# Kernel tuning notes

Hardware: AMD Instinct MI355X
Metric: run time of the kernel (lower is better)

## Reference

```python
import jax, jax.numpy as jnp
import numpy as np

A0, A1, A2 = 1.0, 1.0, 0.5
TEMPERATURE = 1.0

B, H, N, D = 2, 8, 1024, 64


def setup_inputs() -> dict:
    key = jax.random.key(0)
    k1, k2, k3, k4, k5 = jax.random.split(key, 5)
    q = jax.random.normal(k1, (B, H, N, D), dtype=jnp.float32)
    k = jax.random.normal(k2, (B, H, N, D), dtype=jnp.float32)
    v = jax.random.normal(k3, (B, H, N, D), dtype=jnp.float32)
    drop_noise = jax.random.normal(k4, (B, H, N, D), dtype=jnp.float32)
    rpe_matrix = jax.random.normal(k5, (2 * N - 1, D), dtype=jnp.float32)
    return {"q": q, "k": k, "v": v, "drop_noise": drop_noise, "rpe_matrix": rpe_matrix}


def reference(q, k, v, drop_noise, rpe_matrix):
    # Degree-2 Taylor approximation of softmax attention (fastmax):
    #   score_ij = a0 + a1*s_ij + a2*s_ij^2,  s_ij = q_i . k_j + q_i . rpe[i-j+n-1]
    #   o_i = sum_j score_ij * v_j / sum_j score_ij
    # Defaults: mask=False (bidirectional), dropout=0.0 (drop_noise unused),
    # normalize=False, temperature=1.0.
    b, h, n, d = q.shape
    qf = q.reshape(b * h, n, d)
    kf = (k / TEMPERATURE).reshape(b * h, n, d)
    vf = v.reshape(b * h, n, d)

    # dot-product term: (bh, n, n)
    qk = jnp.einsum('bid,bjd->bij', qf, kf)

    # RPE term: P[b,i,r] = q_i . rpe[r]; gather r = i - j + n - 1
    P = jnp.einsum('bid,rd->bir', qf, rpe_matrix)  # (bh, n, 2n-1)
    rel = jnp.arange(n)[:, None] - jnp.arange(n)[None, :] + (n - 1)  # (n, n)
    rel = jnp.broadcast_to(rel[None], (b * h, n, n))
    qk = qk + jnp.take_along_axis(P, rel, axis=2)

    s = A0 + A1 * qk + A2 * qk * qk  # Taylor kernel scores

    denom = jnp.sum(s, axis=-1, keepdims=True)  # (bh, n, 1)
    o = jnp.einsum('bij,bjd->bid', s, vf) / denom
    return o.reshape(b, h, n, d)
```

## Files before the change

kernel.cpp:

```cpp
#include <hip/hip_runtime.h>
#include <hip/hip_bf16.h>


#define NSEQ 1024
#define DH   64
#define BM   64
#define BN   64
#define NBH  16
#define ROWS_TOTAL (NBH * NSEQ)
#define NUM_ELEMS  ((size_t)ROWS_TOTAL * DH)

typedef short bf16x8 __attribute__((ext_vector_type(8)));
typedef float f32x4  __attribute__((ext_vector_type(4)));

__device__ __forceinline__ unsigned short f2bf(float x) {
    return __builtin_bit_cast(unsigned short, __float2bfloat16(x));
}
__device__ __forceinline__ unsigned pack2(float lo, float hi) {
    return (unsigned)f2bf(lo) | ((unsigned)f2bf(hi) << 16);
}
__device__ __forceinline__ unsigned long long pack4(float4 x) {
    unsigned lo = pack2(x.x, x.y), hi = pack2(x.z, x.w);
    return (unsigned long long)lo | ((unsigned long long)hi << 32);
}

template<int JSPLIT>
__global__ __launch_bounds__(512, 2)
void fastmax_kernel(const float* __restrict__ qg, const float* __restrict__ kg,
                    const float* __restrict__ vg, const float* __restrict__ rpe,
                    float* __restrict__ outg, float* __restrict__ wsbuf)
{
    __shared__ __align__(16) unsigned char ldsK[64 * 128];
    __shared__ __align__(16) unsigned char ldsR[128 * 128];
    __shared__ __align__(16) unsigned char ldsVT[64 * 136];
    __shared__ __align__(16) unsigned char ldsS[8 * 16 * 80];

    const int tid = threadIdx.x;
    const int w   = tid >> 6;
    const int l   = tid & 63;
    const int lr  = l & 15;
    const int lg  = l >> 4;
    const int wst = w >> 1;
    const int wj  = w & 1;

    const int b  = blockIdx.x;
    const int js = b % JSPLIT;
    const int it = (b / JSPLIT) & 15;
    const int bh = b / (JSPLIT * 16);
    const int i0 = it * BM;

    const float* qbh = qg + (size_t)bh * (NSEQ * DH);
    const float* kbh = kg + (size_t)bh * (NSEQ * DH);
    const float* vbh = vg + (size_t)bh * (NSEQ * DH);

    bf16x8 qf[2];
    {
        const float* qrow = qbh + (size_t)(i0 + wst * 16 + lr) * DH + lg * 8;
        #pragma unroll
        for (int kc = 0; kc < 2; ++kc) {
            float4 a  = *reinterpret_cast<const float4*>(qrow + kc * 32);
            float4 b4 = *reinterpret_cast<const float4*>(qrow + kc * 32 + 4);
            bf16x8 f;
            f[0] = (short)f2bf(a.x);  f[1] = (short)f2bf(a.y);
            f[2] = (short)f2bf(a.z);  f[3] = (short)f2bf(a.w);
            f[4] = (short)f2bf(b4.x); f[5] = (short)f2bf(b4.y);
            f[6] = (short)f2bf(b4.z); f[7] = (short)f2bf(b4.w);
            qf[kc] = f;
        }
    }

    f32x4 oacc[4];
    #pragma unroll
    for (int dt = 0; dt < 4; ++dt) oacc[dt] = (f32x4){0.f, 0.f, 0.f, 0.f};
    float dp[4] = {0.f, 0.f, 0.f, 0.f};

    unsigned char* myS = ldsS + w * (16 * 80);
    const int t0w = wst * 16 - wj * 32 + 32;

    constexpr int NJT = (NSEQ / BN) / JSPLIT;
    for (int jt = js * NJT; jt < (js + 1) * NJT; ++jt) {
        const int j0  = jt * BN;
        const int rlo = i0 - j0 + 960;

        __syncthreads();

        {
            const float4* src = reinterpret_cast<const float4*>(kbh + (size_t)j0 * DH);
            #pragma unroll
            for (int itr = 0; itr < 2; ++itr) {
                int i = itr * 512 + tid;
                float4 x = src[i];
                int row = i >> 4, colb = (i & 15) * 8;
                *reinterpret_cast<unsigned long long*>(
                    ldsK + ((row * 128 + colb) ^ ((row & 7) << 4))) = pack4(x);
            }
        }
        {
            #pragma unroll
            for (int itr = 0; itr < 4; ++itr) {
                int i = itr * 512 + tid;
                int row = i >> 4;
                int r = rlo + row; if (r > 2 * NSEQ - 2) r = 2 * NSEQ - 2;
                float4 x = reinterpret_cast<const float4*>(rpe)[r * 16 + (i & 15)];
                int colb = (i & 15) * 8;
                *reinterpret_cast<unsigned long long*>(
                    ldsR + ((row * 128 + colb) ^ ((row & 7) << 4))) = pack4(x);
            }
        }
        {
            const float4* src = reinterpret_cast<const float4*>(vbh + (size_t)j0 * DH);
            #pragma unroll
            for (int itr = 0; itr < 2; ++itr) {
                int i = itr * 512 + tid;
                float4 x = src[i];
                int j = i >> 4, d0 = (i & 15) * 4;
                unsigned char* p = ldsVT + j * 2;
                *reinterpret_cast<unsigned short*>(p + (d0 + 0) * 136) = f2bf(x.x);
                *reinterpret_cast<unsigned short*>(p + (d0 + 1) * 136) = f2bf(x.y);
                *reinterpret_cast<unsigned short*>(p + (d0 + 2) * 136) = f2bf(x.z);
                *reinterpret_cast<unsigned short*>(p + (d0 + 3) * 136) = f2bf(x.w);
            }
        }
        __syncthreads();

        f32x4 pacc[3];
        #pragma unroll
        for (int ct = 0; ct < 3; ++ct) pacc[ct] = (f32x4){0.f, 0.f, 0.f, 0.f};
        #pragma unroll
        for (int kc = 0; kc < 2; ++kc) {
            #pragma unroll
            for (int ct = 0; ct < 3; ++ct) {
                int row = t0w + ct * 16 + lr;
                bf16x8 bfrag = *reinterpret_cast<const bf16x8*>(
                    ldsR + ((row * 128 + kc * 64 + lg * 16) ^ ((row & 7) << 4)));
                pacc[ct] = __builtin_amdgcn_mfma_f32_16x16x32_bf16(qf[kc], bfrag, pacc[ct], 0, 0, 0);
            }
        }

        f32x4 sacc[2];
        #pragma unroll
        for (int ct = 0; ct < 2; ++ct) sacc[ct] = (f32x4){0.f, 0.f, 0.f, 0.f};
        #pragma unroll
        for (int kc = 0; kc < 2; ++kc) {
            #pragma unroll
            for (int ct = 0; ct < 2; ++ct) {
                int row = wj * 32 + ct * 16 + lr;
                bf16x8 bfrag = *reinterpret_cast<const bf16x8*>(
                    ldsK + ((row * 128 + kc * 64 + lg * 16) ^ ((row & 7) << 4)));
                sacc[ct] = __builtin_amdgcn_mfma_f32_16x16x32_bf16(qf[kc], bfrag, sacc[ct], 0, 0, 0);
            }
        }

        #pragma unroll
        for (int r = 0; r < 4; ++r) {
            int m = lg * 4 + r;
            int idx = ((l & 48) + ((m - lr + 15) & 15)) << 2;
            int g0 = __builtin_amdgcn_ds_bpermute(idx, __float_as_int(pacc[0][r]));
            int g1 = __builtin_amdgcn_ds_bpermute(idx, __float_as_int(pacc[1][r]));
            int g2 = __builtin_amdgcn_ds_bpermute(idx, __float_as_int(pacc[2][r]));
            bool hi = (m > lr);
            float p0 = __int_as_float(hi ? g2 : g1);
            float p1 = __int_as_float(hi ? g1 : g0);
            float s0 = sacc[0][r] + p0;
            float c0 = fmaf(s0, fmaf(0.5f, s0, 1.0f), 1.0f);
            dp[r] += c0;
            *reinterpret_cast<unsigned short*>(myS + m * 80 + lr * 2) = f2bf(c0);
            float s1 = sacc[1][r] + p1;
            float c1 = fmaf(s1, fmaf(0.5f, s1, 1.0f), 1.0f);
            dp[r] += c1;
            *reinterpret_cast<unsigned short*>(myS + m * 80 + 32 + lr * 2) = f2bf(c1);
        }

        bf16x8 af = *reinterpret_cast<const bf16x8*>(myS + lr * 80 + lg * 16);
        #pragma unroll
        for (int dt = 0; dt < 4; ++dt) {
            const unsigned char* vp = ldsVT + (dt * 16 + lr) * 136 + wj * 64 + lg * 16;
            union { unsigned long long u[2]; bf16x8 v; } bb;
            bb.u[0] = *reinterpret_cast<const unsigned long long*>(vp);
            bb.u[1] = *reinterpret_cast<const unsigned long long*>(vp + 8);
            oacc[dt] = __builtin_amdgcn_mfma_f32_16x16x32_bf16(af, bb.v, oacc[dt], 0, 0, 0);
        }
    }

    #pragma unroll
    for (int r = 0; r < 4; ++r) {
        #pragma unroll
        for (int m = 1; m < 16; m <<= 1) dp[r] += __shfl_xor(dp[r], m, 64);
    }

    if constexpr (JSPLIT == 1) {
        __syncthreads();
        float* ored = reinterpret_cast<float*>(ldsR);
        float* dred = reinterpret_cast<float*>(ldsK);
        if (wj == 1) {
            #pragma unroll
            for (int dt = 0; dt < 4; ++dt) {
                #pragma unroll
                for (int r = 0; r < 4; ++r) {
                    int row = lg * 4 + r;
                    ored[wst * 1024 + row * 64 + dt * 16 + lr] = oacc[dt][r];
                }
            }
            if (lr == 0) {
                #pragma unroll
                for (int r = 0; r < 4; ++r) dred[wst * 16 + lg * 4 + r] = dp[r];
            }
        }
        __syncthreads();
        if (wj == 0) {
            float* ob = outg + (size_t)bh * (NSEQ * DH) + (size_t)(i0 + wst * 16) * DH;
            float rd[4];
            #pragma unroll
            for (int r = 0; r < 4; ++r) {
                int row = lg * 4 + r;
                rd[r] = 1.0f / (dp[r] + dred[wst * 16 + row]);
            }
            #pragma unroll
            for (int dt = 0; dt < 4; ++dt) {
                #pragma unroll
                for (int r = 0; r < 4; ++r) {
                    int row = lg * 4 + r;
                    float num = oacc[dt][r] + ored[wst * 1024 + row * 64 + dt * 16 + lr];
                    ob[row * DH + dt * 16 + lr] = num * rd[r];
                }
            }
        }
    } else {
        const int js2  = js * 2 + wj;
        const int rowg = bh * NSEQ + i0 + wst * 16;
        float* nw = wsbuf + (size_t)js2 * NUM_ELEMS + (size_t)rowg * DH;
        #pragma unroll
        for (int dt = 0; dt < 4; ++dt) {
            #pragma unroll
            for (int r = 0; r < 4; ++r) {
                nw[(lg * 4 + r) * DH + dt * 16 + lr] = oacc[dt][r];
            }
        }
        float* dw = wsbuf + (size_t)(2 * JSPLIT) * NUM_ELEMS + (size_t)js2 * ROWS_TOTAL + rowg;
        if (lr == 0) {
            #pragma unroll
            for (int r = 0; r < 4; ++r) dw[lg * 4 + r] = dp[r];
        }
    }
}

template<int NP>
__global__ __launch_bounds__(256)
void reduce_kernel(const float* __restrict__ wsbuf, float* __restrict__ outg)
{
    const size_t idx  = (size_t)blockIdx.x * 256 + threadIdx.x;
    const size_t flat = idx * 4;
    const int row = (int)(flat >> 6);
    const float* dbase = wsbuf + (size_t)NP * NUM_ELEMS;

    float4 acc = make_float4(0.f, 0.f, 0.f, 0.f);
    float den = 0.f;
    #pragma unroll
    for (int p = 0; p < NP; ++p) {
        float4 x = *reinterpret_cast<const float4*>(wsbuf + (size_t)p * NUM_ELEMS + flat);
        acc.x += x.x; acc.y += x.y; acc.z += x.z; acc.w += x.w;
        den += dbase[(size_t)p * ROWS_TOTAL + row];
    }
    float rdi = 1.0f / den;
    acc.x *= rdi; acc.y *= rdi; acc.z *= rdi; acc.w *= rdi;
    *reinterpret_cast<float4*>(outg + flat) = acc;
}

extern "C" void kernel_launch(void* const* d_in, const int* in_sizes, int n_in,
                              void* d_out, int out_size, void* d_ws, size_t ws_size,
                              hipStream_t stream) {
    const float* q   = (const float*)d_in[0];
    const float* k   = (const float*)d_in[1];
    const float* v   = (const float*)d_in[2];
    const float* rpe = (const float*)d_in[4];
    float* out = (float*)d_out;
    float* wsb = (float*)d_ws;

    auto need = [](int jsplit) -> size_t {
        return ((size_t)(2 * jsplit) * NUM_ELEMS + (size_t)(2 * jsplit) * ROWS_TOTAL)
               * sizeof(float);
    };

    if (ws_size >= need(4)) {
        hipLaunchKernelGGL((fastmax_kernel<4>), dim3(256 * 4), dim3(512), 0, stream,
                           q, k, v, rpe, out, wsb);
        hipLaunchKernelGGL((reduce_kernel<8>), dim3(1024), dim3(256), 0, stream, wsb, out);
    } else if (ws_size >= need(2)) {
        hipLaunchKernelGGL((fastmax_kernel<2>), dim3(256 * 2), dim3(512), 0, stream,
                           q, k, v, rpe, out, wsb);
        hipLaunchKernelGGL((reduce_kernel<4>), dim3(1024), dim3(256), 0, stream, wsb, out);
    } else {
        hipLaunchKernelGGL((fastmax_kernel<1>), dim3(256), dim3(512), 0, stream,
                           q, k, v, rpe, out, wsb);
    }
}
```

Baseline: 102.5 us.

## Double-buffer LDS tiles and prefetch next K/V/RPE tile into registers

Restructures the j-tile loop so global loads for the next K, V and RPE tiles are issued into registers before the current tile's MFMA work. The loaded data is then written into alternating LDS buffers, which removes one barrier per iteration. This hides global memory latency behind compute. In exchange it doubles LDS usage for K/R/V and adds 32 VGPRs of prefetch storage, which may hurt occupancy or cause spills.

```diff
diff --git a/kernel.cpp b/kernel.cpp
--- a/kernel.cpp
+++ b/kernel.cpp
@@ -10,6 +10,10 @@
 #define ROWS_TOTAL (NBH * NSEQ)
 #define NUM_ELEMS  ((size_t)ROWS_TOTAL * DH)
 
+#define SZK 8192
+#define SZR 16384
+#define SZV 8704
+
 typedef short bf16x8 __attribute__((ext_vector_type(8)));
 typedef float f32x4  __attribute__((ext_vector_type(4)));
 
@@ -30,9 +34,9 @@
                     const float* __restrict__ vg, const float* __restrict__ rpe,
                     float* __restrict__ outg, float* __restrict__ wsbuf)
 {
-    __shared__ __align__(16) unsigned char ldsK[64 * 128];
-    __shared__ __align__(16) unsigned char ldsR[128 * 128];
-    __shared__ __align__(16) unsigned char ldsVT[64 * 136];
+    __shared__ __align__(16) unsigned char ldsK[2 * SZK];
+    __shared__ __align__(16) unsigned char ldsR[2 * SZR];
+    __shared__ __align__(16) unsigned char ldsVT[2 * SZV];
     __shared__ __align__(16) unsigned char ldsS[8 * 16 * 80];
 
     const int tid = threadIdx.x;
@@ -78,49 +82,57 @@
     const int t0w = wst * 16 - wj * 32 + 32;
 
     constexpr int NJT = (NSEQ / BN) / JSPLIT;
-    for (int jt = js * NJT; jt < (js + 1) * NJT; ++jt) {
-        const int j0  = jt * BN;
+    const int jt0 = js * NJT;
+
+    float4 pk[2], pr[4], pv[2];
+    auto issue = [&](int jt) {
+        const int j0 = jt * BN;
         const int rlo = i0 - j0 + 960;
-
-        __syncthreads();
-
-        {
-            const float4* src = reinterpret_cast<const float4*>(kbh + (size_t)j0 * DH);
-            #pragma unroll
-            for (int itr = 0; itr < 2; ++itr) {
-                int i = itr * 512 + tid;
-                float4 x = src[i];
-                int row = i >> 4, colb = (i & 15) * 8;
-                *reinterpret_cast<unsigned long long*>(
-                    ldsK + ((row * 128 + colb) ^ ((row & 7) << 4))) = pack4(x);
-            }
-        }
-        {
-            #pragma unroll
-            for (int itr = 0; itr < 4; ++itr) {
-                int i = itr * 512 + tid;
-                int row = i >> 4;
-                int r = rlo + row; if (r > 2 * NSEQ - 2) r = 2 * NSEQ - 2;
-                float4 x = reinterpret_cast<const float4*>(rpe)[r * 16 + (i & 15)];
-                int colb = (i & 15) * 8;
-                *reinterpret_cast<unsigned long long*>(
-                    ldsR + ((row * 128 + colb) ^ ((row & 7) << 4))) = pack4(x);
-            }
-        }
-        {
-            const float4* src = reinterpret_cast<const float4*>(vbh + (size_t)j0 * DH);
-            #pragma unroll
-            for (int itr = 0; itr < 2; ++itr) {
-                int i = itr * 512 + tid;
-                float4 x = src[i];
-                int j = i >> 4, d0 = (i & 15) * 4;
-                unsigned char* p = ldsVT + j * 2;
-                *reinterpret_cast<unsigned short*>(p + (d0 + 0) * 136) = f2bf(x.x);
-                *reinterpret_cast<unsigned short*>(p + (d0 + 1) * 136) = f2bf(x.y);
-                *reinterpret_cast<unsigned short*>(p + (d0 + 2) * 136) = f2bf(x.z);
-                *reinterpret_cast<unsigned short*>(p + (d0 + 3) * 136) = f2bf(x.w);
-            }
-        }
+        const float4* sK = reinterpret_cast<const float4*>(kbh + (size_t)j0 * DH);
+        const float4* sV = reinterpret_cast<const float4*>(vbh + (size_t)j0 * DH);
+        pk[0] = sK[tid]; pk[1] = sK[512 + tid];
+        pv[0] = sV[tid]; pv[1] = sV[512 + tid];
+        #pragma unroll
+        for (int itr = 0; itr < 4; ++itr) {
+            int i = itr * 512 + tid;
+            int row = i >> 4;
+            int r = rlo + row; if (r > 2 * NSEQ - 2) r = 2 * NSEQ - 2;
+            pr[itr] = reinterpret_cast<const float4*>(rpe)[r * 16 + (i & 15)];
+        }
+    };
+    issue(jt0);
+
+    for (int ii = 0; ii < NJT; ++ii) {
+        unsigned char* bK = ldsK + (ii & 1) * SZK;
+        unsigned char* bR = ldsR + (ii & 1) * SZR;
+        unsigned char* bV = ldsVT + (ii & 1) * SZV;
+
+        #pragma unroll
+        for (int itr = 0; itr < 2; ++itr) {
+            int i = itr * 512 + tid;
+            int row = i >> 4, colb = (i & 15) * 8;
+            *reinterpret_cast<unsigned long long*>(
+                bK + ((row * 128 + colb) ^ ((row & 7) << 4))) = pack4(pk[itr]);
+        }
+        #pragma unroll
+        for (int itr = 0; itr < 4; ++itr) {
+            int i = itr * 512 + tid;
+            int row = i >> 4, colb = (i & 15) * 8;
+            *reinterpret_cast<unsigned long long*>(
+                bR + ((row * 128 + colb) ^ ((row & 7) << 4))) = pack4(pr[itr]);
+        }
+        #pragma unroll
+        for (int itr = 0; itr < 2; ++itr) {
+            int i = itr * 512 + tid;
+            int j = i >> 4, d0 = (i & 15) * 4;
+            unsigned char* p = bV + j * 2;
+            *reinterpret_cast<unsigned short*>(p + (d0 + 0) * 136) = f2bf(pv[itr].x);
+            *reinterpret_cast<unsigned short*>(p + (d0 + 1) * 136) = f2bf(pv[itr].y);
+            *reinterpret_cast<unsigned short*>(p + (d0 + 2) * 136) = f2bf(pv[itr].z);
+            *reinterpret_cast<unsigned short*>(p + (d0 + 3) * 136) = f2bf(pv[itr].w);
+        }
+        if (ii + 1 < NJT) issue(jt0 + ii + 1);
+
         __syncthreads();
 
         f32x4 pacc[3];
@@ -132,7 +144,7 @@
             for (int ct = 0; ct < 3; ++ct) {
                 int row = t0w + ct * 16 + lr;
                 bf16x8 bfrag = *reinterpret_cast<const bf16x8*>(
-                    ldsR + ((row * 128 + kc * 64 + lg * 16) ^ ((row & 7) << 4)));
+                    bR + ((row * 128 + kc * 64 + lg * 16) ^ ((row & 7) << 4)));
                 pacc[ct] = __builtin_amdgcn_mfma_f32_16x16x32_bf16(qf[kc], bfrag, pacc[ct], 0, 0, 0);
             }
         }
@@ -146,7 +158,7 @@
             for (int ct = 0; ct < 2; ++ct) {
                 int row = wj * 32 + ct * 16 + lr;
                 bf16x8 bfrag = *reinterpret_cast<const bf16x8*>(
-                    ldsK + ((row * 128 + kc * 64 + lg * 16) ^ ((row & 7) << 4)));
+                    bK + ((row * 128 + kc * 64 + lg * 16) ^ ((row & 7) << 4)));
                 sacc[ct] = __builtin_amdgcn_mfma_f32_16x16x32_bf16(qf[kc], bfrag, sacc[ct], 0, 0, 0);
             }
         }
@@ -174,7 +186,7 @@
         bf16x8 af = *reinterpret_cast<const bf16x8*>(myS + lr * 80 + lg * 16);
         #pragma unroll
         for (int dt = 0; dt < 4; ++dt) {
-            const unsigned char* vp = ldsVT + (dt * 16 + lr) * 136 + wj * 64 + lg * 16;
+            const unsigned char* vp = bV + (dt * 16 + lr) * 136 + wj * 64 + lg * 16;
             union { unsigned long long u[2]; bf16x8 v; } bb;
             bb.u[0] = *reinterpret_cast<const unsigned long long*>(vp);
             bb.u[1] = *reinterpret_cast<const unsigned long long*>(vp + 8);
```

Result: slower. 106.7 us (+4.1%).
